# Optimization experiments

Hardware: AMD Instinct MI355X
Metric: run time of the kernel (lower is better)

Reference implementation:

```python
import jax, jax.numpy as jnp
import numpy as np

BATCH, NUM_MASKS, IN_DIM, OUT_DIM = 512, 16, 1024, 1024


def setup_inputs() -> dict:
    key = jax.random.key(0)
    k1, k2, k3 = jax.random.split(key, 3)
    x = jax.random.normal(k1, (BATCH, NUM_MASKS, IN_DIM), dtype=jnp.float32)
    kernel = jax.random.normal(k2, (IN_DIM, OUT_DIM), dtype=jnp.float32) * (1.0 / np.sqrt(IN_DIM))
    masks = jax.random.uniform(k3, (NUM_MASKS, IN_DIM, OUT_DIM), dtype=jnp.float32)
    return {"x": x, "kernel": kernel, "masks": masks}


def reference(x, kernel, masks):
    # masked_kernel[m, i, o] = kernel[i, o] * masks[m, i, o]
    masked_kernel = kernel[None, :, :] * masks  # (M, I, O)
    # Original tf.scan serializes batch; equivalent math is one batched einsum:
    # out[b, m, o] = sum_i x[b, m, i] * masked_kernel[m, i, o]
    # NOTE: the executed tf.scan path applies NO activation, so neither do we.
    out = jnp.einsum('bmi,mio->bmo', x, masked_kernel)  # (B, M, O)
    return out
```

## Files before the change

kernel.cpp:

```cpp
#include <hip/hip_runtime.h>
#include <hip/hip_bf16.h>


#define BATCH 512
#define NMASK 16
#define IN_D  1024
#define OUT_D 1024

using bf16x8 = __attribute__((ext_vector_type(8))) __bf16;
using bf16x4 = __attribute__((ext_vector_type(4))) __bf16;
using f32x16 = __attribute__((ext_vector_type(16))) float;
using f32x4  = __attribute__((ext_vector_type(4))) float;
using f32x2  = __attribute__((ext_vector_type(2))) float;

typedef const __attribute__((address_space(1))) void gvoid_t;
typedef __attribute__((address_space(3))) void lvoid_t;

__device__ __forceinline__ void dma16(const void* g, const void* l) {
    __builtin_amdgcn_global_load_lds((gvoid_t*)(uintptr_t)g,
                                     (lvoid_t*)(uintptr_t)l, 16, 0, 0);
}

__global__ void __launch_bounds__(512, 4)
mdl_prep(const float* __restrict__ X,
         const float* __restrict__ Kn,
         const float* __restrict__ Mk,
         unsigned short* __restrict__ Wt,
         unsigned short* __restrict__ Xp)
{
    const int t   = threadIdx.x;
    const int bid = blockIdx.x;

    if (bid < 2048) {
        const int l = t & 63;
        const int w = t >> 6;
        const int wg = (bid & 7) * 256 + (bid >> 3);
        const int m  = wg >> 7;
        const int ob = (wg >> 4) & 7;
        const int k2 = wg & 15;

        const int i0 = k2 * 64 + w * 8;
        const int o0 = ob * 128 + 2 * l;

        const float* mkb = Mk + ((size_t)m * IN_D + i0) * OUT_D + o0;
        const float* knb = Kn + (size_t)i0 * OUT_D + o0;

        f32x2 a[8], b[8];
#pragma unroll
        for (int r = 0; r < 8; ++r) {
            a[r] = *(const f32x2*)(mkb + (size_t)r * OUT_D);
            b[r] = *(const f32x2*)(knb + (size_t)r * OUT_D);
        }
        bf16x8 g0, g1;
#pragma unroll
        for (int r = 0; r < 8; ++r) {
            g0[r] = (__bf16)(a[r][0] * b[r][0]);
            g1[r] = (__bf16)(a[r][1] * b[r][1]);
        }
        unsigned short* dst = Wt + (size_t)wg * 8192 + t * 16;
        *(bf16x8*)(dst)     = g0;
        *(bf16x8*)(dst + 8) = g1;
    } else {
        const int b2    = bid - 2048;
        const int strip = b2 >> 2;
        const int Gq    = b2 & 3;
        const int m  = strip >> 3;
        const int bt = strip & 7;
        const int row = t >> 3;
        const int oc  = t & 7;

        const float* src = X + ((size_t)(bt * 64 + row) * NMASK + m) * IN_D
                             + Gq * 256 + oc * 32;
        f32x4 av[8];
#pragma unroll
        for (int q = 0; q < 8; ++q)
            av[q] = *(const f32x4*)(src + q * 4);

        unsigned short* dstS = Xp + (size_t)strip * 65536
                                  + (size_t)(Gq * 32 + oc * 4) * 512 + row * 8;
#pragma unroll
        for (int j = 0; j < 4; ++j) {
            bf16x8 g;
#pragma unroll
            for (int e = 0; e < 4; ++e) {
                g[e]     = (__bf16)av[2 * j][e];
                g[4 + e] = (__bf16)av[2 * j + 1][e];
            }
            *(bf16x8*)(dstS + (size_t)j * 512) = g;
        }
    }
}

struct Frags { bf16x8 a[2][2]; bf16x8 b[2][2]; };

__global__ void __launch_bounds__(256, 2)
mdl_gemm2(const unsigned short* __restrict__ Xp,
          const unsigned short* __restrict__ Wt,
          float* __restrict__ Out)
{
    const int t = threadIdx.x;
    const int l = t & 63;
    const int w = t >> 6;

    const int raw = blockIdx.x;
    const int wg  = (raw & 7) * 64 + (raw >> 3);
    const int v   = wg * 4 + w;
    const int m   = v >> 7;
    const int v7  = v & 127;
    const int bt  = v7 >> 4;
    const int ot  = v7 & 15;

    const unsigned short* Ap = Xp + (size_t)(m * 8 + bt) * 65536;
    const unsigned short* Bp = Wt + (size_t)(m * 8 + (ot >> 1)) * 131072
                                  + (size_t)((ot & 1) * 64) * 8;

    const int la = (l & 31) * 8;
    const int ls = l >> 5;

    f32x16 acc[2][2];
#pragma unroll
    for (int ti = 0; ti < 2; ++ti)
#pragma unroll
        for (int tj = 0; tj < 2; ++tj)
#pragma unroll
            for (int e = 0; e < 16; ++e)
                acc[ti][tj][e] = 0.f;

    auto LOADF = [&](Frags& F, int kb) {
#pragma unroll
        for (int s = 0; s < 2; ++s) {
            const int G = (kb >> 3) + s * 2 + ls;
            const unsigned short* ab = Ap + (size_t)G * 512 + la;
            F.a[s][0] = *(const bf16x8*)(ab);
            F.a[s][1] = *(const bf16x8*)(ab + 256);
            const unsigned short* bb = Bp + (size_t)(G >> 3) * 8192
                                          + (size_t)(G & 7) * 1024 + la;
            F.b[s][0] = *(const bf16x8*)(bb);
            F.b[s][1] = *(const bf16x8*)(bb + 256);
        }
    };
    auto MF = [&](Frags& F) {
#pragma unroll
        for (int s = 0; s < 2; ++s)
#pragma unroll
            for (int ti = 0; ti < 2; ++ti)
#pragma unroll
                for (int tj = 0; tj < 2; ++tj)
                    acc[ti][tj] = __builtin_amdgcn_mfma_f32_32x32x16_bf16(
                        F.a[s][ti], F.b[s][tj], acc[ti][tj], 0, 0, 0);
    };

    Frags S0, S1;
    LOADF(S0, 0);
    for (int kb = 0; kb < IN_D; kb += 64) {
        LOADF(S1, kb + 32);
        __builtin_amdgcn_sched_barrier(0);
        MF(S0);
        LOADF(S0, (kb + 64) & (IN_D - 1));
        __builtin_amdgcn_sched_barrier(0);
        MF(S1);
    }

    const int r0 = bt * 64 + 4 * ls;
    const int c0 = ot * 64 + (l & 31);
#pragma unroll
    for (int ti = 0; ti < 2; ++ti) {
#pragma unroll
        for (int tj = 0; tj < 2; ++tj) {
#pragma unroll
            for (int g = 0; g < 4; ++g) {
#pragma unroll
                for (int q = 0; q < 4; ++q) {
                    const int row = r0 + ti * 32 + g * 8 + q;
                    const int col = c0 + tj * 32;
                    Out[((size_t)row * NMASK + m) * OUT_D + col] =
                        acc[ti][tj][g * 4 + q];
                }
            }
        }
    }
}

#define FAKP 40
#define FBKP 34
#define FMFSZ (32 * 128)

__global__ void __launch_bounds__(512, 4)
mdl_fused_fallback(const float* __restrict__ X,
                   const float* __restrict__ Kn,
                   const float* __restrict__ Mk,
                   float* __restrict__ Out)
{
    __shared__ __align__(16) float          Mf[3 * FMFSZ];
    __shared__ __align__(16) unsigned short As[128 * FAKP];
    __shared__ __align__(16) unsigned short Bs[128 * FBKP];

    const int t = threadIdx.x;
    const int l = t & 63;
    const int w = t >> 6;

    const int raw = blockIdx.x;
    const int wg  = (raw & 7) * 64 + (raw >> 3);
    const int m   = wg >> 5;
    const int ob  = (wg >> 2) & 7;
    const int bb  = wg & 3;

    const int wr = w >> 2, wc = w & 3;

    f32x4 acc[4][2];
#pragma unroll
    for (int mi = 0; mi < 4; ++mi)
#pragma unroll
        for (int ni = 0; ni < 2; ++ni)
            acc[mi][ni] = (f32x4){0.f, 0.f, 0.f, 0.f};

    const int a_row = t >> 2;
    const int a_kh  = (t & 3) * 8;
    const int o2 = (t & 63) * 2;
    const int k4 = w * 4;

    const int obase = ob * 128;
    const float* Xa  = X + ((size_t)(bb * 128 + a_row) * NMASK + m) * IN_D + a_kh;
    const float* Knb = Kn + obase + o2;
    const float* Mkm = Mk + (size_t)m * IN_D * OUT_D;

    auto DMA = [&](int tile, int c) {
        const int kt = tile * 32;
#pragma unroll
        for (int j = 0; j < 2; ++j) {
            const int k = j * 16 + w * 2 + (l >> 5);
            const float* gsrc = Mkm + (size_t)(kt + k) * OUT_D + obase + (l & 31) * 4;
            dma16(gsrc, &Mf[c * FMFSZ + j * 2048 + w * 256]);
        }
    };

    DMA(0, 0);
    DMA(1, 1);
    asm volatile("s_waitcnt vmcnt(2)" ::: "memory");
    __builtin_amdgcn_sched_barrier(0);
    __builtin_amdgcn_s_barrier();
    __builtin_amdgcn_sched_barrier(0);

    int c_cur = 0, c_nxt = 1, c_far = 2;

    for (int tt = 0; tt < 32; ++tt) {
        const int kt = tt * 32;
        f32x4 xv0 = *(const f32x4*)(Xa + kt);
        f32x4 xv1 = *(const f32x4*)(Xa + kt + 4);
        f32x2 kv[4];
#pragma unroll
        for (int r = 0; r < 4; ++r)
            kv[r] = *(const f32x2*)(Knb + (size_t)(kt + k4 + r) * OUT_D);
        __builtin_amdgcn_sched_barrier(0);
        DMA((tt + 2 < 32) ? tt + 2 : 0, c_far);
        __builtin_amdgcn_sched_barrier(0);
        {
            f32x2 mvv[4];
#pragma unroll
            for (int r = 0; r < 4; ++r)
                mvv[r] = *(const f32x2*)(&Mf[c_cur * FMFSZ + (k4 + r) * 128 + o2]);
#pragma unroll
            for (int c = 0; c < 2; ++c) {
                bf16x4 vv;
#pragma unroll
                for (int r = 0; r < 4; ++r)
                    vv[r] = (__bf16)(kv[r][c] * mvv[r][c]);
                *(bf16x4*)(&Bs[(o2 + c) * FBKP + k4]) = vv;
            }
            bf16x8 va;
#pragma unroll
            for (int j = 0; j < 4; ++j) {
                va[j] = (__bf16)xv0[j]; va[4 + j] = (__bf16)xv1[j];
            }
            *(bf16x8*)(&As[a_row * FAKP + a_kh]) = va;
        }
        asm volatile("s_waitcnt lgkmcnt(0)" ::: "memory");
        __builtin_amdgcn_sched_barrier(0);
        __builtin_amdgcn_s_barrier();
        __builtin_amdgcn_sched_barrier(0);
        {
            const int kg = (l >> 4) * 8;
            bf16x8 bfv[2];
#pragma unroll
            for (int ni = 0; ni < 2; ++ni) {
                const int n = wc * 32 + ni * 16 + (l & 15);
                bf16x4 lo = *(const bf16x4*)(&Bs[n * FBKP + kg]);
                bf16x4 hi = *(const bf16x4*)(&Bs[n * FBKP + kg + 4]);
                bf16x8 f;
                f[0] = lo[0]; f[1] = lo[1]; f[2] = lo[2]; f[3] = lo[3];
                f[4] = hi[0]; f[5] = hi[1]; f[6] = hi[2]; f[7] = hi[3];
                bfv[ni] = f;
            }
#pragma unroll
            for (int mi = 0; mi < 4; ++mi) {
                const int r = wr * 64 + mi * 16 + (l & 15);
                bf16x8 af = *(const bf16x8*)(&As[r * FAKP + kg]);
#pragma unroll
                for (int ni = 0; ni < 2; ++ni)
                    acc[mi][ni] = __builtin_amdgcn_mfma_f32_16x16x32_bf16(
                        af, bfv[ni], acc[mi][ni], 0, 0, 0);
            }
        }
        asm volatile("s_waitcnt vmcnt(2)" ::: "memory");
        __builtin_amdgcn_sched_barrier(0);
        __builtin_amdgcn_s_barrier();
        __builtin_amdgcn_sched_barrier(0);
        const int tmp = c_cur; c_cur = c_nxt; c_nxt = c_far; c_far = tmp;
    }
    asm volatile("s_waitcnt vmcnt(0)" ::: "memory");

    const int r0 = bb * 128 + wr * 64 + (l >> 4) * 4;
    const int c0 = ob * 128 + wc * 32 + (l & 15);
#pragma unroll
    for (int mi = 0; mi < 4; ++mi) {
#pragma unroll
        for (int j = 0; j < 4; ++j) {
            const size_t row = (size_t)(r0 + mi * 16 + j);
            float* op = Out + (row * NMASK + m) * OUT_D + c0;
#pragma unroll
            for (int ni = 0; ni < 2; ++ni)
                op[ni * 16] = acc[mi][ni][j];
        }
    }
}

extern "C" void kernel_launch(void* const* d_in, const int* in_sizes, int n_in,
                              void* d_out, int out_size, void* d_ws, size_t ws_size,
                              hipStream_t stream) {
    (void)in_sizes; (void)n_in; (void)out_size;
    const float* X  = (const float*)d_in[0];
    const float* Kn = (const float*)d_in[1];
    const float* Mk = (const float*)d_in[2];
    float* Out = (float*)d_out;

    const size_t w_bytes = (size_t)NMASK * IN_D * OUT_D * sizeof(unsigned short);
    const size_t x_bytes = (size_t)BATCH * NMASK * IN_D * sizeof(unsigned short);

    if (ws_size >= w_bytes + x_bytes) {
        unsigned short* Wt = (unsigned short*)d_ws;
        unsigned short* Xp = (unsigned short*)d_ws + w_bytes / 2;
        mdl_prep<<<2560, 512, 0, stream>>>(X, Kn, Mk, Wt, Xp);
        mdl_gemm2<<<512, 256, 0, stream>>>(Xp, Wt, Out);
    } else {
        mdl_fused_fallback<<<512, 512, 0, stream>>>(X, Kn, Mk, Out);
    }
}
```

Measured before the change: 60.89 us.

## Repack masked weight buffer by k-group and column for wider prep loads

Changes the bf16 packed weight layout to index by (mask, k-group of 8, output column). The prep kernel now reads float4 per row instead of float2 and writes four bf16x8 vectors per thread, so it needs half as many blocks. The GEMM computes B fragment addresses directly from the new layout. The goal is more efficient global loads in the bandwidth-bound prep stage. The cost is that B fragment reads in the GEMM now hit a different address pattern, and their coalescing may change.

```diff
diff --git a/kernel.cpp b/kernel.cpp
--- a/kernel.cpp
+++ b/kernel.cpp
@@ -31,37 +31,37 @@
     const int t   = threadIdx.x;
     const int bid = blockIdx.x;
 
-    if (bid < 2048) {
-        const int l = t & 63;
-        const int w = t >> 6;
-        const int wg = (bid & 7) * 256 + (bid >> 3);
-        const int m  = wg >> 7;
-        const int ob = (wg >> 4) & 7;
-        const int k2 = wg & 15;
-
-        const int i0 = k2 * 64 + w * 8;
-        const int o0 = ob * 128 + 2 * l;
-
-        const float* mkb = Mk + ((size_t)m * IN_D + i0) * OUT_D + o0;
-        const float* knb = Kn + (size_t)i0 * OUT_D + o0;
-
-        f32x2 a[8], b[8];
+    if (bid < 1024) {
+        const int wg = (bid & 7) * 128 + (bid >> 3);
+        const int m  = wg >> 6;
+        const int G2 = wg & 63;
+        const int g01 = t >> 8;
+        const int oc  = t & 255;
+        const int col0 = oc * 4;
+        const int G = G2 * 2 + g01;
+        const int i0 = G * 8;
+
+        const float* mkb = Mk + ((size_t)m * IN_D + i0) * OUT_D + col0;
+        const float* knb = Kn + (size_t)i0 * OUT_D + col0;
+
+        f32x4 a[8], b[8];
 #pragma unroll
         for (int r = 0; r < 8; ++r) {
-            a[r] = *(const f32x2*)(mkb + (size_t)r * OUT_D);
-            b[r] = *(const f32x2*)(knb + (size_t)r * OUT_D);
-        }
-        bf16x8 g0, g1;
-#pragma unroll
-        for (int r = 0; r < 8; ++r) {
-            g0[r] = (__bf16)(a[r][0] * b[r][0]);
-            g1[r] = (__bf16)(a[r][1] * b[r][1]);
-        }
-        unsigned short* dst = Wt + (size_t)wg * 8192 + t * 16;
-        *(bf16x8*)(dst)     = g0;
-        *(bf16x8*)(dst + 8) = g1;
+            a[r] = *(const f32x4*)(mkb + (size_t)r * OUT_D);
+            b[r] = *(const f32x4*)(knb + (size_t)r * OUT_D);
+        }
+        unsigned short* dst =
+            Wt + (((size_t)m * 128 + G) * 1024 + col0) * 8;
+#pragma unroll
+        for (int c = 0; c < 4; ++c) {
+            bf16x8 g;
+#pragma unroll
+            for (int r = 0; r < 8; ++r)
+                g[r] = (__bf16)(a[r][c] * b[r][c]);
+            *(bf16x8*)(dst + c * 8) = g;
+        }
     } else {
-        const int b2    = bid - 2048;
+        const int b2    = bid - 1024;
         const int strip = b2 >> 2;
         const int Gq    = b2 & 3;
         const int m  = strip >> 3;
@@ -111,11 +111,9 @@
     const int ot  = v7 & 15;
 
     const unsigned short* Ap = Xp + (size_t)(m * 8 + bt) * 65536;
-    const unsigned short* Bp = Wt + (size_t)(m * 8 + (ot >> 1)) * 131072
-                                  + (size_t)((ot & 1) * 64) * 8;
-
     const int la = (l & 31) * 8;
     const int ls = l >> 5;
+    const int bcol = ot * 64 + (l & 31);
 
     f32x16 acc[2][2];
 #pragma unroll
@@ -133,8 +131,8 @@
             const unsigned short* ab = Ap + (size_t)G * 512 + la;
             F.a[s][0] = *(const bf16x8*)(ab);
             F.a[s][1] = *(const bf16x8*)(ab + 256);
-            const unsigned short* bb = Bp + (size_t)(G >> 3) * 8192
-                                          + (size_t)(G & 7) * 1024 + la;
+            const unsigned short* bb =
+                Wt + (((size_t)m * 128 + G) * 1024 + bcol) * 8;
             F.b[s][0] = *(const bf16x8*)(bb);
             F.b[s][1] = *(const bf16x8*)(bb + 256);
         }
@@ -339,7 +337,7 @@
     if (ws_size >= w_bytes + x_bytes) {
         unsigned short* Wt = (unsigned short*)d_ws;
         unsigned short* Xp = (unsigned short*)d_ws + w_bytes / 2;
-        mdl_prep<<<2560, 512, 0, stream>>>(X, Kn, Mk, Wt, Xp);
+        mdl_prep<<<1536, 512, 0, stream>>>(X, Kn, Mk, Wt, Xp);
         mdl_gemm2<<<512, 256, 0, stream>>>(Xp, Wt, Out);
     } else {
         mdl_fused_fallback<<<512, 512, 0, stream>>>(X, Kn, Mk, Out);
```

Result: no change. 60.86 us (-0.0%).
